# Optimization experiments

Measured on AMD Instinct MI355X. Metric: run time of the kernel, lower is better.

The kernel has to match this reference:

```python
import jax, jax.numpy as jnp
import numpy as np

B, T, N, D, H, NMASK = 8192, 2, 40, 64, 1, 3
EPS = 1e-5


def setup_inputs() -> dict:
    key = jax.random.key(0)
    ks = jax.random.split(key, 12)
    F = T * N * 2 * D  # flattened feature size fed to BatchNorm1d
    return {
        "x": jax.random.normal(ks[0], (B, N, D), jnp.float32),
        "masker": jax.random.uniform(ks[1], (T, NMASK, N, N), jnp.float32, -0.27, 0.27),  # xavier-like
        "ln_gamma": jnp.ones((N,), jnp.float32),
        "ln_beta": jnp.zeros((N,), jnp.float32),
        "gnn_w": jax.random.normal(ks[2], (1, T, H, 2 * D, D), jnp.float32) * 0.05,
        "gnn_b": jax.random.normal(ks[3], (T, H, N, D), jnp.float32) * 0.05,
        "bn_gamma": jnp.ones((H, F), jnp.float32),
        "bn_beta": jnp.zeros((H, F), jnp.float32),
        "bn_mean": jax.random.normal(ks[4], (H, F), jnp.float32) * 0.1,
        "bn_var": jax.random.uniform(ks[5], (H, F), jnp.float32, 0.5, 1.5),
        "gate_w": jax.random.normal(ks[6], (N * D, N), jnp.float32) * 0.02,
        "gate_b": jnp.zeros((N,), jnp.float32),
    }


def reference(x, masker, ln_gamma, ln_beta, gnn_w, gnn_b, bn_gamma, bn_beta, bn_mean, bn_var, gate_w, gate_b):
    b = x.shape[0]
    # broadcast input to towers: (B, T, N, D)
    h = jnp.broadcast_to(x[:, None], (b, T, N, D))
    # adjacency from product of mask matrices: (T, N, N)
    adj = jax.nn.relu(jnp.prod(masker, axis=1))
    mask = (adj != 0).astype(x.dtype)
    # LayerNorm(num_fields) applied on transposed adj == normalize over rows (axis -2)
    mu = adj.mean(axis=-2, keepdims=True)
    var = adj.var(axis=-2, keepdims=True)
    ln = (adj - mu) / jnp.sqrt(var + EPS) * ln_gamma[:, None] + ln_beta[:, None]
    x_masked = ln + (1.0 - mask) * (-1e9) + jnp.eye(N, dtype=x.dtype)
    # softmax over rows (dim=1 of (T,N,N)) then re-mask
    A = jax.nn.softmax(x_masked, axis=1) * mask  # (T, N, N)
    for idx in range(H):
        # nei[b,t,n,d] = sum_m h[b,t,m,d] * A[t,m,n]
        nei = jnp.einsum('btmd,tmn->btnd', h, A)
        hc = jnp.concatenate([h, nei], axis=-1)  # (B,T,N,2D)
        flat = hc.reshape(b, -1)
        flat = (flat - bn_mean[idx]) / jnp.sqrt(bn_var[idx] + EPS) * bn_gamma[idx] + bn_beta[idx]
        hc = flat.reshape(b, T, N, 2 * D)
        # per-tower transform: (B,T,N,2D) x (T,2D,D) -> (B,T,N,D)
        h = jnp.einsum('btnf,tfd->btnd', hc, gnn_w[0, :, idx]) + gnn_b[:, idx]
    # attention pooling over fields
    logits = h.reshape(b, T, N * D) @ gate_w + gate_b  # (B,T,N)
    w = jax.nn.softmax(logits, axis=2)
    return jnp.sum(h * w[..., None], axis=2)  # (B, T, D)
```

## Files before the change

### kernel.cpp

```cpp
#include <hip/hip_runtime.h>
#include <hip/hip_bf16.h>
#include <stdint.h>

typedef float v4f __attribute__((ext_vector_type(4)));
typedef short v8s __attribute__((ext_vector_type(8)));
typedef union { v8s v; unsigned u[4]; } v8u;

#define NB 40

__device__ __forceinline__ unsigned short f2b(float f) {
  __hip_bfloat16 h = __float2bfloat16(f);
  unsigned short u;
  __builtin_memcpy(&u, &h, 2);
  return u;
}
__device__ __forceinline__ unsigned pk2(float lo, float hi) {
  __hip_bfloat162 h = __float22bfloat162_rn(make_float2(lo, hi));
  unsigned u;
  __builtin_memcpy(&u, &h, 4);
  return u;
}
__device__ __forceinline__ float b2f16(unsigned short h) {
  return __uint_as_float(((unsigned)h) << 16);
}
__device__ __forceinline__ float blo(unsigned u) { return __uint_as_float(u << 16); }
__device__ __forceinline__ float bhi(unsigned u) { return __uint_as_float(u & 0xFFFF0000u); }


__global__ __launch_bounds__(256) void prep(
    const float* __restrict__ masker,
    const float* __restrict__ ln_gamma, const float* __restrict__ ln_beta,
    const float* __restrict__ gnn_w, const float* __restrict__ gnn_b,
    const float* __restrict__ bn_gamma, const float* __restrict__ bn_beta,
    const float* __restrict__ bn_mean, const float* __restrict__ bn_var,
    const float* __restrict__ gate_w,
    unsigned short* __restrict__ A1pk, unsigned short* __restrict__ W2pk,
    unsigned short* __restrict__ Gpk, float* __restrict__ s1,
    float* __restrict__ sNT, float* __restrict__ bias2T)
{
  const int tid = threadIdx.x;
  if (blockIdx.x == 0) {
    __shared__ float AtL[2 * NB * NB];
    const int w = tid >> 6, lane = tid & 63;
    #pragma unroll 1
    for (int it = 0; it < 20; ++it) {
      const int c = it * 4 + w;
      const int t = c / NB, n = c % NB;
      const int m = lane;
      float adj = 0.f;
      if (m < NB) {
        float p = masker[((t*3+0)*NB+m)*NB+n]
                * masker[((t*3+1)*NB+m)*NB+n]
                * masker[((t*3+2)*NB+m)*NB+n];
        adj = p > 0.f ? p : 0.f;
      }
      float s = adj;
      #pragma unroll
      for (int d = 1; d < 64; d <<= 1) s += __shfl_xor(s, d);
      const float mu = s * (1.f/NB);
      const float dv = (m < NB) ? adj - mu : 0.f;
      float v2 = dv * dv;
      #pragma unroll
      for (int d = 1; d < 64; d <<= 1) v2 += __shfl_xor(v2, d);
      const float inv = rsqrtf(v2 * (1.f/NB) + 1e-5f);
      float val = -3.0e38f;
      if (m < NB) {
        float lnv = dv * inv * ln_gamma[m] + ln_beta[m];
        val = lnv + (adj != 0.f ? 0.f : -1e9f) + (m == n ? 1.f : 0.f);
      }
      float mx = val;
      #pragma unroll
      for (int d = 1; d < 64; d <<= 1) mx = fmaxf(mx, __shfl_xor(mx, d));
      const float e = (m < NB) ? __expf(val - mx) : 0.f;
      float es = e;
      #pragma unroll
      for (int d = 1; d < 64; d <<= 1) es += __shfl_xor(es, d);
      if (m < NB)
        AtL[(t*NB+n)*NB + m] = (adj != 0.f) ? e / es : 0.f;
    }
    __syncthreads();
    for (int e = tid; e < 6144; e += 256) {
      int frag = e >> 9, rem = e & 511, lane2 = rem >> 3, jj = rem & 7;
      int t = frag / 6, r2 = frag % 6, nt = r2 >> 1, ks = r2 & 1;
      int n = nt*16 + (lane2 & 15);
      int m = ks*32 + (lane2 >> 4)*8 + jj;
      A1pk[e] = f2b((n < NB && m < NB) ? AtL[(t*NB+n)*NB+m] : 0.f);
    }
  } else {
    const int gid = (blockIdx.x - 1) * 256 + tid, gsz = 63 * 256;
    for (int e = gid; e < 16384; e += gsz) {
      int frag = e >> 9, rem = e & 511, lane = rem >> 3, jj = rem & 7;
      int t = frag >> 4, ks = (frag >> 2) & 3, dt = frag & 3;
      int f = ks*32 + (lane >> 4)*8 + jj, d = dt*16 + (lane & 15);
      W2pk[e] = f2b(gnn_w[t*8192 + f*64 + d]);
    }
    for (int e = gid; e < 122880; e += gsz) {
      int frag = e >> 9, rem = e & 511, lane = rem >> 3, jj = rem & 7;
      int kt = frag / 3, jt = frag % 3;
      int flp = kt*32 + (lane >> 4)*8 + jj;
      int dd = flp / 40, nn = flp - dd*40;
      int j = jt*16 + (lane & 15);
      Gpk[e] = f2b(j < NB ? gate_w[(nn*64 + dd)*NB + j] : 0.f);
    }
    for (int e = gid; e < 5120; e += gsz) {
      int t = e / 2560, n = (e % 2560) / 64, d = e & 63;
      int F = (t*NB + n)*128 + d;
      s1[e] = bn_gamma[F] * rsqrtf(bn_var[F] + 1e-5f);
    }
    for (int e = gid; e < 5120; e += gsz) {
      int t = e / 2560, d = (e % 2560) / 40, n = e % 40;
      int F = (t*NB + n)*128 + 64 + d;
      sNT[e] = bn_gamma[F] * rsqrtf(bn_var[F] + 1e-5f);
    }
    for (int e4 = gid; e4 < 20480; e4 += gsz) {
      int e = e4 >> 2, part = e4 & 3;
      int t = e / 2560, d = (e % 2560) / 40, n = e % 40;
      float acc = (part == 0) ? gnn_b[(t*NB + n)*64 + d] : 0.f;
      int Fb = (t*NB + n)*128;
      int f0 = part * 32;
      for (int f = f0; f < f0 + 32; ++f) {
        float s = bn_gamma[Fb+f] * rsqrtf(bn_var[Fb+f] + 1e-5f);
        float o = bn_beta[Fb+f] - bn_mean[Fb+f] * s;
        acc += o * gnn_w[t*8192 + f*64 + d];
      }
      acc += __shfl_xor(acc, 1);
      acc += __shfl_xor(acc, 2);
      if (part == 0) bias2T[e] = acc;
    }
  }
}

__global__ __launch_bounds__(256) void kernelA(
    const float* __restrict__ x,
    const unsigned short* __restrict__ A1pk, const unsigned short* __restrict__ W2pk,
    const float* __restrict__ s1, const float* __restrict__ sNT,
    const float* __restrict__ bias2T, unsigned short* __restrict__ hLg)
{
  __shared__ __align__(16) unsigned short sh[4*5760 + 576];

  const int tid = threadIdx.x;
  const int lane = tid & 63;
  const int w = tid >> 6;
  const int l15 = lane & 15, q = lane >> 4;
  const int b = blockIdx.x * 4 + w;

  unsigned short* Uw  = sh + w * 5760;
  unsigned short* Vw  = Uw + 2880;
  unsigned short* xTw = Vw;

  const float* xb = x + (size_t)b * 2560;
  v8s b1[4][2];

  #pragma unroll 1
  for (int t = 0; t < 2; ++t) {
    #pragma unroll
    for (int it = 0; it < 5; ++it) {
      const int n  = it*8 + (lane >> 3);
      const int f0 = (lane & 7) * 8;
      const float* xp = xb + n*64 + f0;
      const float4 fA = *(const float4*)xp;
      const float4 fB = *(const float4*)(xp + 4);
      const float* sp = s1 + (t*NB + n)*64 + f0;
      const float4 sA = *(const float4*)sp;
      const float4 sB = *(const float4*)(sp + 4);
      uint4 p;
      p.x = pk2(fA.x*sA.x, fA.y*sA.y);
      p.y = pk2(fA.z*sA.z, fA.w*sA.w);
      p.z = pk2(fB.x*sB.x, fB.y*sB.y);
      p.w = pk2(fB.z*sB.z, fB.w*sB.w);
      *(uint4*)(Uw + n*72 + f0) = p;
      if (t == 0) {
        xTw[(f0+0)*42 + n] = f2b(fA.x);
        xTw[(f0+1)*42 + n] = f2b(fA.y);
        xTw[(f0+2)*42 + n] = f2b(fA.z);
        xTw[(f0+3)*42 + n] = f2b(fA.w);
        xTw[(f0+4)*42 + n] = f2b(fB.x);
        xTw[(f0+5)*42 + n] = f2b(fB.y);
        xTw[(f0+6)*42 + n] = f2b(fB.z);
        xTw[(f0+7)*42 + n] = f2b(fB.w);
      }
    }
    if (t == 0) {
      #pragma unroll
      for (int dt = 0; dt < 4; ++dt) {
        const int r = dt*16 + l15;
        const unsigned* p0 = (const unsigned*)(xTw + r*42 + q*8);
        v8u u0;
        u0.u[0] = p0[0]; u0.u[1] = p0[1]; u0.u[2] = p0[2]; u0.u[3] = p0[3];
        b1[dt][0] = u0.v;
        v8s bk1 = {0,0,0,0,0,0,0,0};
        if (q == 0) {
          const unsigned* p1 = (const unsigned*)(xTw + r*42 + 32);
          v8u u1;
          u1.u[0] = p1[0]; u1.u[1] = p1[1]; u1.u[2] = p1[2]; u1.u[3] = p1[3];
          bk1 = u1.v;
        }
        b1[dt][1] = bk1;
      }
    }
    v8s a1[3][2];
    #pragma unroll
    for (int nt = 0; nt < 3; ++nt)
      #pragma unroll
      for (int ks = 0; ks < 2; ++ks)
        a1[nt][ks] = *(const v8s*)(A1pk + (((t*3 + nt)*2 + ks) << 9) + lane*8);
    #pragma unroll
    for (int nt = 0; nt < 3; ++nt) {
      #pragma unroll
      for (int dt = 0; dt < 4; ++dt) {
        v4f acc = {0.f, 0.f, 0.f, 0.f};
        acc = __builtin_amdgcn_mfma_f32_16x16x32_bf16(a1[nt][0], b1[dt][0], acc, 0, 0, 0);
        acc = __builtin_amdgcn_mfma_f32_16x16x32_bf16(a1[nt][1], b1[dt][1], acc, 0, 0, 0);
        const int d = dt*16 + l15;
        const float4 sv = *(const float4*)(sNT + (t*64 + d)*40 + nt*16 + q*4);
        #pragma unroll
        for (int r = 0; r < 4; ++r) {
          const int n = nt*16 + q*4 + r;
          if (n < NB) Vw[n*72 + d] = f2b(acc[r]*sv[r]);
        }
      }
    }
    v8s af[3][4];
    #pragma unroll
    for (int nt = 0; nt < 3; ++nt) {
      const unsigned short* rowU = Uw + (nt*16 + l15)*72;
      const unsigned short* rowV = Vw + (nt*16 + l15)*72;
      af[nt][0] = *(const v8s*)(rowU + q*8);
      af[nt][1] = *(const v8s*)(rowU + 32 + q*8);
      af[nt][2] = *(const v8s*)(rowV + q*8);
      af[nt][3] = *(const v8s*)(rowV + 32 + q*8);
    }
    unsigned short* hLb = hLg + ((size_t)b*2 + t)*2560;
    #pragma unroll
    for (int dt = 0; dt < 4; ++dt) {
      v4f a2[3] = {{0,0,0,0},{0,0,0,0},{0,0,0,0}};
      #pragma unroll
      for (int ks = 0; ks < 4; ++ks) {
        const v8s w2k = *(const v8s*)(W2pk + ((t*16 + ks*4 + dt) << 9) + lane*8);
        #pragma unroll
        for (int nt = 0; nt < 3; ++nt)
          a2[nt] = __builtin_amdgcn_mfma_f32_16x16x32_bf16(af[nt][ks], w2k, a2[nt], 0, 0, 0);
      }
      const int d = dt*16 + l15;
      #pragma unroll
      for (int nt = 0; nt < 3; ++nt) {
        const int n0 = nt*16 + q*4;
        if (n0 < NB) {
          const float4 bv = *(const float4*)(bias2T + (t*64 + d)*40 + n0);
          uint2 pr;
          pr.x = pk2(a2[nt][0] + bv.x, a2[nt][1] + bv.y);
          pr.y = pk2(a2[nt][2] + bv.z, a2[nt][3] + bv.w);
          *(uint2*)(hLb + d*40 + n0) = pr;
        }
      }
    }
  }
}

__global__ __launch_bounds__(512) void kernelB(
    const unsigned short* __restrict__ hLg, const unsigned short* __restrict__ Gpk,
    const float* __restrict__ gate_b, float* __restrict__ out)
{
  __shared__ float pj[8 * 48 * 17];
  __shared__ float wgt[2 * 16 * NB];

  const int tid = threadIdx.x;
  const int w = tid >> 6, lane = tid & 63;
  const int l = lane & 15, q = lane >> 4;
  const int b0 = blockIdx.x * 16;

  v4f ac[2][3];
  #pragma unroll
  for (int t = 0; t < 2; ++t)
    #pragma unroll
    for (int jt = 0; jt < 3; ++jt)
      ac[t][jt] = (v4f){0.f, 0.f, 0.f, 0.f};

  const unsigned short* hb = hLg + (size_t)(b0 + l) * 2 * 2560 + q * 8;
  int kt = w;
  v8s g0 = *(const v8s*)(Gpk + ((kt*3+0) << 9) + lane*8);
  v8s g1 = *(const v8s*)(Gpk + ((kt*3+1) << 9) + lane*8);
  v8s g2 = *(const v8s*)(Gpk + ((kt*3+2) << 9) + lane*8);
  v8s bf0 = *(const v8s*)(hb + kt*32);
  v8s bf1 = *(const v8s*)(hb + 2560 + kt*32);
  #pragma unroll
  for (int i = 0; i < 10; ++i) {
    const int ktn = kt + 8;
    v8s ng0, ng1, ng2, nbf0, nbf1;
    if (i < 9) {
      ng0  = *(const v8s*)(Gpk + ((ktn*3+0) << 9) + lane*8);
      ng1  = *(const v8s*)(Gpk + ((ktn*3+1) << 9) + lane*8);
      ng2  = *(const v8s*)(Gpk + ((ktn*3+2) << 9) + lane*8);
      nbf0 = *(const v8s*)(hb + ktn*32);
      nbf1 = *(const v8s*)(hb + 2560 + ktn*32);
    }
    ac[0][0] = __builtin_amdgcn_mfma_f32_16x16x32_bf16(g0, bf0, ac[0][0], 0, 0, 0);
    ac[0][1] = __builtin_amdgcn_mfma_f32_16x16x32_bf16(g1, bf0, ac[0][1], 0, 0, 0);
    ac[0][2] = __builtin_amdgcn_mfma_f32_16x16x32_bf16(g2, bf0, ac[0][2], 0, 0, 0);
    ac[1][0] = __builtin_amdgcn_mfma_f32_16x16x32_bf16(g0, bf1, ac[1][0], 0, 0, 0);
    ac[1][1] = __builtin_amdgcn_mfma_f32_16x16x32_bf16(g1, bf1, ac[1][1], 0, 0, 0);
    ac[1][2] = __builtin_amdgcn_mfma_f32_16x16x32_bf16(g2, bf1, ac[1][2], 0, 0, 0);
    g0 = ng0; g1 = ng1; g2 = ng2; bf0 = nbf0; bf1 = nbf1;
    kt = ktn;
  }

  #pragma unroll
  for (int t = 0; t < 2; ++t) {
    if (t) __syncthreads();
    #pragma unroll
    for (int jt = 0; jt < 3; ++jt)
      #pragma unroll
      for (int r = 0; r < 4; ++r)
        pj[(w*48 + jt*16 + q*4 + r)*17 + l] = ac[t][jt][r];
    __syncthreads();
    #pragma unroll
    for (int hb2 = 0; hb2 < 2; ++hb2) {
      const int bb = w*2 + hb2;
      float v = -3.0e38f;
      if (lane < NB) {
        v = gate_b[lane];
        #pragma unroll
        for (int w8 = 0; w8 < 8; ++w8) v += pj[(w8*48 + lane)*17 + bb];
      }
      float mx = v;
      #pragma unroll
      for (int m = 1; m < 64; m <<= 1) mx = fmaxf(mx, __shfl_xor(mx, m));
      const float e = (lane < NB) ? __expf(v - mx) : 0.f;
      float es = e;
      #pragma unroll
      for (int m = 1; m < 64; m <<= 1) es += __shfl_xor(es, m);
      if (lane < NB) wgt[(t*16 + bb)*NB + lane] = e / es;
    }
  }
  __syncthreads();
  {
    const int bb = tid >> 5, t = (tid >> 4) & 1, d0 = (tid & 15) * 4;
    const uint4* hp4 = (const uint4*)(hLg + ((size_t)(b0 + bb)*2 + t)*2560 + d0*40);
    const float* wb = wgt + (t*16 + bb)*NB;
    float s[4] = {0.f, 0.f, 0.f, 0.f};
    #pragma unroll
    for (int k = 0; k < 20; ++k) {
      const uint4 rr = hp4[k];
      const int e0 = k*8;
      s[(e0+0)/40] += blo(rr.x)*wb[(e0+0)%40]; s[(e0+1)/40] += bhi(rr.x)*wb[(e0+1)%40];
      s[(e0+2)/40] += blo(rr.y)*wb[(e0+2)%40]; s[(e0+3)/40] += bhi(rr.y)*wb[(e0+3)%40];
      s[(e0+4)/40] += blo(rr.z)*wb[(e0+4)%40]; s[(e0+5)/40] += bhi(rr.z)*wb[(e0+5)%40];
      s[(e0+6)/40] += blo(rr.w)*wb[(e0+6)%40]; s[(e0+7)/40] += bhi(rr.w)*wb[(e0+7)%40];
    }
    float4 ov = make_float4(s[0], s[1], s[2], s[3]);
    *(float4*)(out + ((size_t)(b0 + bb)*2 + t)*64 + d0) = ov;
  }
}

extern "C" void kernel_launch(void* const* d_in, const int* in_sizes, int n_in,
                              void* d_out, int out_size, void* d_ws, size_t ws_size,
                              hipStream_t stream) {
  const float* x        = (const float*)d_in[0];
  const float* masker   = (const float*)d_in[1];
  const float* ln_gamma = (const float*)d_in[2];
  const float* ln_beta  = (const float*)d_in[3];
  const float* gnn_w    = (const float*)d_in[4];
  const float* gnn_b    = (const float*)d_in[5];
  const float* bn_gamma = (const float*)d_in[6];
  const float* bn_beta  = (const float*)d_in[7];
  const float* bn_mean  = (const float*)d_in[8];
  const float* bn_var   = (const float*)d_in[9];
  const float* gate_w   = (const float*)d_in[10];
  const float* gate_b   = (const float*)d_in[11];
  float* out = (float*)d_out;

  char* ws = (char*)d_ws;
  unsigned short* A1pk   = (unsigned short*)(ws + 0);
  unsigned short* W2pk   = (unsigned short*)(ws + 12288);
  unsigned short* Gpk    = (unsigned short*)(ws + 45056);
  float*          s1     = (float*)(ws + 290816);
  float*          sNT    = (float*)(ws + 311296);
  float*          bias2T = (float*)(ws + 331904);
  unsigned short* hLg    = (unsigned short*)(ws + 352512);

  prep<<<64, 256, 0, stream>>>(masker, ln_gamma, ln_beta, gnn_w, gnn_b,
                               bn_gamma, bn_beta, bn_mean, bn_var, gate_w,
                               A1pk, W2pk, Gpk, s1, sNT, bias2T);
  kernelA<<<2048, 256, 0, stream>>>(x, A1pk, W2pk, s1, sNT, bias2T, hLg);
  kernelB<<<512, 512, 0, stream>>>(hLg, Gpk, gate_b, out);
}
```

Measured before the change: 271.3 us.

## Load MFMA operands directly from global, drop LDS staging, deepen kernelB prefetch

In kernelA the x-transpose and the scaled-x (U) tiles are no longer staged through shared memory. MFMA operand fragments are now built directly from global loads into registers, which halves the per-wave LDS footprint and removes the LDS round trips. The x transpose now comes from strided scalar global loads, which may coalesce poorly. kernelB's software pipeline is changed from single- to double-buffered prefetch of the G and h fragments, at the cost of more registers.

```diff
diff --git a/kernel.cpp b/kernel.cpp
--- a/kernel.cpp
+++ b/kernel.cpp
@@ -136,7 +136,7 @@
     const float* __restrict__ s1, const float* __restrict__ sNT,
     const float* __restrict__ bias2T, unsigned short* __restrict__ hLg)
 {
-  __shared__ __align__(16) unsigned short sh[4*5760 + 576];
+  __shared__ __align__(16) unsigned short sh[4*2880 + 576];
 
   const int tid = threadIdx.x;
   const int lane = tid & 63;
@@ -144,66 +144,67 @@
   const int l15 = lane & 15, q = lane >> 4;
   const int b = blockIdx.x * 4 + w;
 
-  unsigned short* Uw  = sh + w * 5760;
-  unsigned short* Vw  = Uw + 2880;
-  unsigned short* xTw = Vw;
-
+  unsigned short* Vw = sh + w * 2880;
   const float* xb = x + (size_t)b * 2560;
+
   v8s b1[4][2];
+  #pragma unroll
+  for (int dt = 0; dt < 4; ++dt) {
+    const int d = dt*16 + l15;
+    v8u u0;
+    #pragma unroll
+    for (int j2 = 0; j2 < 4; ++j2)
+      u0.u[j2] = pk2(xb[(q*8 + 2*j2    )*64 + d],
+                     xb[(q*8 + 2*j2 + 1)*64 + d]);
+    b1[dt][0] = u0.v;
+    v8s bk1 = {0,0,0,0,0,0,0,0};
+    if (q == 0) {
+      v8u u1;
+      #pragma unroll
+      for (int j2 = 0; j2 < 4; ++j2)
+        u1.u[j2] = pk2(xb[(32 + 2*j2    )*64 + d],
+                       xb[(32 + 2*j2 + 1)*64 + d]);
+      bk1 = u1.v;
+    }
+    b1[dt][1] = bk1;
+  }
 
   #pragma unroll 1
   for (int t = 0; t < 2; ++t) {
-    #pragma unroll
-    for (int it = 0; it < 5; ++it) {
-      const int n  = it*8 + (lane >> 3);
-      const int f0 = (lane & 7) * 8;
-      const float* xp = xb + n*64 + f0;
-      const float4 fA = *(const float4*)xp;
-      const float4 fB = *(const float4*)(xp + 4);
-      const float* sp = s1 + (t*NB + n)*64 + f0;
-      const float4 sA = *(const float4*)sp;
-      const float4 sB = *(const float4*)(sp + 4);
-      uint4 p;
-      p.x = pk2(fA.x*sA.x, fA.y*sA.y);
-      p.y = pk2(fA.z*sA.z, fA.w*sA.w);
-      p.z = pk2(fB.x*sB.x, fB.y*sB.y);
-      p.w = pk2(fB.z*sB.z, fB.w*sB.w);
-      *(uint4*)(Uw + n*72 + f0) = p;
-      if (t == 0) {
-        xTw[(f0+0)*42 + n] = f2b(fA.x);
-        xTw[(f0+1)*42 + n] = f2b(fA.y);
-        xTw[(f0+2)*42 + n] = f2b(fA.z);
-        xTw[(f0+3)*42 + n] = f2b(fA.w);
-        xTw[(f0+4)*42 + n] = f2b(fB.x);
-        xTw[(f0+5)*42 + n] = f2b(fB.y);
-        xTw[(f0+6)*42 + n] = f2b(fB.z);
-        xTw[(f0+7)*42 + n] = f2b(fB.w);
-      }
-    }
-    if (t == 0) {
-      #pragma unroll
-      for (int dt = 0; dt < 4; ++dt) {
-        const int r = dt*16 + l15;
-        const unsigned* p0 = (const unsigned*)(xTw + r*42 + q*8);
-        v8u u0;
-        u0.u[0] = p0[0]; u0.u[1] = p0[1]; u0.u[2] = p0[2]; u0.u[3] = p0[3];
-        b1[dt][0] = u0.v;
-        v8s bk1 = {0,0,0,0,0,0,0,0};
-        if (q == 0) {
-          const unsigned* p1 = (const unsigned*)(xTw + r*42 + 32);
-          v8u u1;
-          u1.u[0] = p1[0]; u1.u[1] = p1[1]; u1.u[2] = p1[2]; u1.u[3] = p1[3];
-          bk1 = u1.v;
-        }
-        b1[dt][1] = bk1;
-      }
-    }
     v8s a1[3][2];
     #pragma unroll
     for (int nt = 0; nt < 3; ++nt)
       #pragma unroll
       for (int ks = 0; ks < 2; ++ks)
         a1[nt][ks] = *(const v8s*)(A1pk + (((t*3 + nt)*2 + ks) << 9) + lane*8);
+
+    v8s uf[3][2];
+    #pragma unroll
+    for (int nt = 0; nt < 3; ++nt) {
+      const int n = nt*16 + l15;
+      if (nt < 2 || l15 < 8) {
+        const float* xp = xb + n*64;
+        const float* sp = s1 + (t*NB + n)*64;
+        #pragma unroll
+        for (int ks = 0; ks < 2; ++ks) {
+          const int f0 = ks*32 + q*8;
+          const float4 xa = *(const float4*)(xp + f0);
+          const float4 xc = *(const float4*)(xp + f0 + 4);
+          const float4 sa = *(const float4*)(sp + f0);
+          const float4 sc = *(const float4*)(sp + f0 + 4);
+          v8u uu;
+          uu.u[0] = pk2(xa.x*sa.x, xa.y*sa.y);
+          uu.u[1] = pk2(xa.z*sa.z, xa.w*sa.w);
+          uu.u[2] = pk2(xc.x*sc.x, xc.y*sc.y);
+          uu.u[3] = pk2(xc.z*sc.z, xc.w*sc.w);
+          uf[nt][ks] = uu.v;
+        }
+      } else {
+        uf[nt][0] = (v8s){0,0,0,0,0,0,0,0};
+        uf[nt][1] = (v8s){0,0,0,0,0,0,0,0};
+      }
+    }
+
     #pragma unroll
     for (int nt = 0; nt < 3; ++nt) {
       #pragma unroll
@@ -220,16 +221,15 @@
         }
       }
     }
-    v8s af[3][4];
+
+    v8s af[3][2];
     #pragma unroll
     for (int nt = 0; nt < 3; ++nt) {
-      const unsigned short* rowU = Uw + (nt*16 + l15)*72;
       const unsigned short* rowV = Vw + (nt*16 + l15)*72;
-      af[nt][0] = *(const v8s*)(rowU + q*8);
-      af[nt][1] = *(const v8s*)(rowU + 32 + q*8);
-      af[nt][2] = *(const v8s*)(rowV + q*8);
-      af[nt][3] = *(const v8s*)(rowV + 32 + q*8);
-    }
+      af[nt][0] = *(const v8s*)(rowV + q*8);
+      af[nt][1] = *(const v8s*)(rowV + 32 + q*8);
+    }
+
     unsigned short* hLb = hLg + ((size_t)b*2 + t)*2560;
     #pragma unroll
     for (int dt = 0; dt < 4; ++dt) {
@@ -237,9 +237,12 @@
       #pragma unroll
       for (int ks = 0; ks < 4; ++ks) {
         const v8s w2k = *(const v8s*)(W2pk + ((t*16 + ks*4 + dt) << 9) + lane*8);
-        #pragma unroll
-        for (int nt = 0; nt < 3; ++nt)
-          a2[nt] = __builtin_amdgcn_mfma_f32_16x16x32_bf16(af[nt][ks], w2k, a2[nt], 0, 0, 0);
+        const v8s aop0 = (ks == 0) ? uf[0][ks] : (ks == 1) ? uf[0][1] : af[0][ks-2];
+        const v8s aop1 = (ks == 0) ? uf[1][ks] : (ks == 1) ? uf[1][1] : af[1][ks-2];
+        const v8s aop2 = (ks == 0) ? uf[2][ks] : (ks == 1) ? uf[2][1] : af[2][ks-2];
+        a2[0] = __builtin_amdgcn_mfma_f32_16x16x32_bf16(aop0, w2k, a2[0], 0, 0, 0);
+        a2[1] = __builtin_amdgcn_mfma_f32_16x16x32_bf16(aop1, w2k, a2[1], 0, 0, 0);
+        a2[2] = __builtin_amdgcn_mfma_f32_16x16x32_bf16(aop2, w2k, a2[2], 0, 0, 0);
       }
       const int d = dt*16 + l15;
       #pragma unroll
@@ -277,31 +280,35 @@
       ac[t][jt] = (v4f){0.f, 0.f, 0.f, 0.f};
 
   const unsigned short* hb = hLg + (size_t)(b0 + l) * 2 * 2560 + q * 8;
-  int kt = w;
-  v8s g0 = *(const v8s*)(Gpk + ((kt*3+0) << 9) + lane*8);
-  v8s g1 = *(const v8s*)(Gpk + ((kt*3+1) << 9) + lane*8);
-  v8s g2 = *(const v8s*)(Gpk + ((kt*3+2) << 9) + lane*8);
-  v8s bf0 = *(const v8s*)(hb + kt*32);
-  v8s bf1 = *(const v8s*)(hb + 2560 + kt*32);
+  v8s g0[2], g1[2], g2[2], bf0[2], bf1[2];
+  #pragma unroll
+  for (int s = 0; s < 2; ++s) {
+    const int kt = w + s*8;
+    g0[s]  = *(const v8s*)(Gpk + ((kt*3+0) << 9) + lane*8);
+    g1[s]  = *(const v8s*)(Gpk + ((kt*3+1) << 9) + lane*8);
+    g2[s]  = *(const v8s*)(Gpk + ((kt*3+2) << 9) + lane*8);
+    bf0[s] = *(const v8s*)(hb + kt*32);
+    bf1[s] = *(const v8s*)(hb + 2560 + kt*32);
+  }
   #pragma unroll
   for (int i = 0; i < 10; ++i) {
-    const int ktn = kt + 8;
-    v8s ng0, ng1, ng2, nbf0, nbf1;
-    if (i < 9) {
-      ng0  = *(const v8s*)(Gpk + ((ktn*3+0) << 9) + lane*8);
-      ng1  = *(const v8s*)(Gpk + ((ktn*3+1) << 9) + lane*8);
-      ng2  = *(const v8s*)(Gpk + ((ktn*3+2) << 9) + lane*8);
-      nbf0 = *(const v8s*)(hb + ktn*32);
-      nbf1 = *(const v8s*)(hb + 2560 + ktn*32);
-    }
-    ac[0][0] = __builtin_amdgcn_mfma_f32_16x16x32_bf16(g0, bf0, ac[0][0], 0, 0, 0);
-    ac[0][1] = __builtin_amdgcn_mfma_f32_16x16x32_bf16(g1, bf0, ac[0][1], 0, 0, 0);
-    ac[0][2] = __builtin_amdgcn_mfma_f32_16x16x32_bf16(g2, bf0, ac[0][2], 0, 0, 0);
-    ac[1][0] = __builtin_amdgcn_mfma_f32_16x16x32_bf16(g0, bf1, ac[1][0], 0, 0, 0);
-    ac[1][1] = __builtin_amdgcn_mfma_f32_16x16x32_bf16(g1, bf1, ac[1][1], 0, 0, 0);
-    ac[1][2] = __builtin_amdgcn_mfma_f32_16x16x32_bf16(g2, bf1, ac[1][2], 0, 0, 0);
-    g0 = ng0; g1 = ng1; g2 = ng2; bf0 = nbf0; bf1 = nbf1;
-    kt = ktn;
+    const int cur = i & 1;
+    const v8s G0 = g0[cur], G1 = g1[cur], G2 = g2[cur];
+    const v8s B0 = bf0[cur], B1 = bf1[cur];
+    if (i < 8) {
+      const int ktn = w + (i+2)*8;
+      g0[cur]  = *(const v8s*)(Gpk + ((ktn*3+0) << 9) + lane*8);
+      g1[cur]  = *(const v8s*)(Gpk + ((ktn*3+1) << 9) + lane*8);
+      g2[cur]  = *(const v8s*)(Gpk + ((ktn*3+2) << 9) + lane*8);
+      bf0[cur] = *(const v8s*)(hb + ktn*32);
+      bf1[cur] = *(const v8s*)(hb + 2560 + ktn*32);
+    }
+    ac[0][0] = __builtin_amdgcn_mfma_f32_16x16x32_bf16(G0, B0, ac[0][0], 0, 0, 0);
+    ac[0][1] = __builtin_amdgcn_mfma_f32_16x16x32_bf16(G1, B0, ac[0][1], 0, 0, 0);
+    ac[0][2] = __builtin_amdgcn_mfma_f32_16x16x32_bf16(G2, B0, ac[0][2], 0, 0, 0);
+    ac[1][0] = __builtin_amdgcn_mfma_f32_16x16x32_bf16(G0, B1, ac[1][0], 0, 0, 0);
+    ac[1][1] = __builtin_amdgcn_mfma_f32_16x16x32_bf16(G1, B1, ac[1][1], 0, 0, 0);
+    ac[1][2] = __builtin_amdgcn_mfma_f32_16x16x32_bf16(G2, B1, ac[1][2], 0, 0, 0);
   }
 
   #pragma unroll
```

Result: slower. 277.6 us (+2.3%).
